# Kernel optimization log

Measured on AMD Instinct MI355X. Metric: run time of the kernel, lower is better.

The kernel has to match this reference:

```python
import jax, jax.numpy as jnp
import numpy as np

B, S, D, H = 8, 1024, 1024, 16
DH = D // H  # 64


def setup_inputs() -> dict:
    key0 = jax.random.key(0)
    ks = jax.random.split(key0, 12)
    mk = lambda k, shape: jax.random.normal(k, shape, dtype=jnp.float32)
    inp = {
        "key": mk(ks[0], (B, S, D)),
        "value": mk(ks[1], (B, S, D)),
        "query": mk(ks[2], (B, S, D)),
        "mask": jax.random.randint(ks[3], (B, S, S), 0, 2).astype(jnp.bool_),
        "Wq": mk(ks[4], (D, D)) * 0.02, "bq": jnp.zeros((D,), jnp.float32),
        "Wk": mk(ks[5], (D, D)) * 0.02, "bk": jnp.zeros((D,), jnp.float32),
        "Wv": mk(ks[6], (D, D)) * 0.02, "bv": jnp.zeros((D,), jnp.float32),
        "Wo": mk(ks[7], (D, D)) * 0.02, "bo": jnp.zeros((D,), jnp.float32),
    }
    return inp


def _split_heads(x):
    # [B, S, D] -> [B, H, S, DH]
    return x.reshape(B, -1, H, DH).transpose(0, 2, 1, 3)


def reference(key, value, query, mask, Wq, bq, Wk, bk, Wv, bv, Wo, bo):
    # linear projections (nn.Linear: x @ W.T + b)
    q = _split_heads(query @ Wq.T + bq) / jnp.sqrt(jnp.float32(DH))
    k = _split_heads(key @ Wk.T + bk)
    v = _split_heads(value @ Wv.T + bv)
    # scores: [B, H, Q, K]
    scores = jnp.einsum("bhqd,bhkd->bhqk", q, k)
    scores = jnp.where(mask[:, None, :, :], jnp.float32(-1e18), scores)
    attn = jax.nn.softmax(scores, axis=-1)
    # dropout is identity in eval mode (deterministic reference)
    ctx = jnp.einsum("bhqk,bhkd->bhqd", attn, v)
    ctx = ctx.transpose(0, 2, 1, 3).reshape(B, -1, D)
    out = ctx @ Wo.T + bo
    return out, attn
```

## Files before the change

### kernel.cpp

```cpp
#include <hip/hip_runtime.h>
#include <hip/hip_bf16.h>

#define BB 8
#define SS 1024
#define DD 1024
#define HH 16
#define DHH 64
#define MM (BB*SS)

typedef __attribute__((ext_vector_type(8))) short short8;
typedef __attribute__((ext_vector_type(4))) float f32x4;
typedef __fp16 half2v __attribute__((ext_vector_type(2)));
typedef __fp16 half8 __attribute__((ext_vector_type(8)));

typedef __attribute__((address_space(3))) void lds_void;
typedef const __attribute__((address_space(1))) void gbl_void;

__device__ __forceinline__ unsigned short f2bf(float f) {
  union { __hip_bfloat16 b; unsigned short u; } cv;
  cv.b = __float2bfloat16(f);
  return cv.u;
}
__device__ __forceinline__ float bf2f(unsigned short u) {
  return __builtin_bit_cast(float, (unsigned)u << 16);
}

__global__ void k_conv_w(const float* __restrict__ in, unsigned short* __restrict__ out,
                         float scale, int n8) {
  int i = blockIdx.x * blockDim.x + threadIdx.x;
  if (i >= n8) return;
  const float4* in4 = (const float4*)in;
  float4 a = in4[i * 2];
  float4 b = in4[i * 2 + 1];
  unsigned int w[4];
  w[0] = f2bf(a.x * scale) | ((unsigned)f2bf(a.y * scale) << 16);
  w[1] = f2bf(a.z * scale) | ((unsigned)f2bf(a.w * scale) << 16);
  w[2] = f2bf(b.x * scale) | ((unsigned)f2bf(b.y * scale) << 16);
  w[3] = f2bf(b.z * scale) | ((unsigned)f2bf(b.w * scale) << 16);
  *(uint4*)(out + (size_t)i * 8) = *(uint4*)w;
}

__global__ void k_detect_mask(const unsigned int* __restrict__ m, int* __restrict__ flag) {
  if (threadIdx.x || blockIdx.x) return;
  int i32 = 1, f32m = 1;
  for (int i = 0; i < 64; ++i) {
    unsigned v = m[i];
    if (v > 1u) i32 = 0;
    if (v != 0u && v != 0x3F800000u) f32m = 0;
  }
  *flag = i32 ? 0 : (f32m ? 1 : 2);
}

__global__ void k_maskbits(const void* __restrict__ mask, const int* __restrict__ mmode,
                           unsigned short* __restrict__ out) {
  int i = blockIdx.x * blockDim.x + threadIdx.x;
  if (i >= BB * 32 * 64 * 32) return;
  int r = i & 31, cb = (i >> 5) & 63, qb = (i >> 11) & 31, b = i >> 16;
  size_t src = ((size_t)(b * SS + qb * 32 + r) * SS) + cb * 16;
  int mm = *mmode;
  unsigned short bits = 0;
  if (mm == 2) {
    const unsigned char* p = (const unsigned char*)mask + src;
    uint4 v = *(const uint4*)p;
    const unsigned char* bytes = (const unsigned char*)&v;
#pragma unroll
    for (int c = 0; c < 16; c++) bits |= (bytes[c] ? 1u : 0u) << c;
  } else {
    const unsigned int* p = (const unsigned int*)mask + src;
#pragma unroll
    for (int q = 0; q < 4; q++) {
      uint4 v = *(const uint4*)(p + q * 4);
      bits |= (v.x ? 1u : 0u) << (q * 4 + 0);
      bits |= (v.y ? 1u : 0u) << (q * 4 + 1);
      bits |= (v.z ? 1u : 0u) << (q * 4 + 2);
      bits |= (v.w ? 1u : 0u) << (q * 4 + 3);
    }
  }
  out[i] = bits;
}

__global__ void __launch_bounds__(256, 2) k_gemm_qkv(
    const unsigned short* __restrict__ Xq, const unsigned short* __restrict__ Xk,
    const unsigned short* __restrict__ Xv,
    const unsigned short* __restrict__ Wqb, const unsigned short* __restrict__ Wkb,
    const unsigned short* __restrict__ Wvb,
    const float* __restrict__ bq, const float* __restrict__ bk, const float* __restrict__ bv,
    unsigned short* __restrict__ Oq, unsigned short* __restrict__ Ok,
    unsigned short* __restrict__ Ov) {
  int z = blockIdx.z;
  const unsigned short* A = (z == 0) ? Xq : (z == 1 ? Xk : Xv);
  const unsigned short* W = (z == 0) ? Wqb : (z == 1 ? Wkb : Wvb);
  const float* bias = (z == 0) ? bq : (z == 1 ? bk : bv);
  float bsc = (z == 0) ? 0.125f : 1.0f;
  unsigned short* O = (z == 0) ? Oq : (z == 1 ? Ok : Ov);

  __shared__ alignas(16) unsigned char As[128 * 64 * 2];
  __shared__ alignas(16) unsigned char Bs[128 * 64 * 2];

  int t = threadIdx.x;
  int row0 = blockIdx.y * 128, col0 = blockIdx.x * 128;
  int w = t >> 6, lane = t & 63, lr = lane & 15, lg = lane >> 4;
  int wm = w >> 1, wn = w & 1;

  int srow = w * 8 + (lane >> 3);
  int scol = (lane & 7) * 8;

  f32x4 z4 = {0.f, 0.f, 0.f, 0.f};
  f32x4 acc[4][4];
#pragma unroll
  for (int m = 0; m < 4; m++)
#pragma unroll
    for (int n = 0; n < 4; n++) acc[m][n] = z4;

  for (int kt = 0; kt < 16; ++kt) {
    int k0 = kt * 64;
#pragma unroll
    for (int i = 0; i < 4; ++i) {
      int r = i * 32 + srow;
      __builtin_amdgcn_global_load_lds(
          (gbl_void*)(A + (size_t)(row0 + r) * DD + k0 + scol),
          (lds_void*)(As + (i * 32 + w * 8) * 128), 16, 0, 0);
      __builtin_amdgcn_global_load_lds(
          (gbl_void*)(W + (size_t)(col0 + r) * DD + k0 + scol),
          (lds_void*)(Bs + (i * 32 + w * 8) * 128), 16, 0, 0);
    }
    __syncthreads();
#pragma unroll
    for (int kk = 0; kk < 2; ++kk) {
      short8 af[4], bfr[4];
#pragma unroll
      for (int m = 0; m < 4; m++) {
        int r = wm * 64 + m * 16 + lr;
        af[m] = *(const short8*)(As + r * 128 + kk * 64 + lg * 16);
      }
#pragma unroll
      for (int n = 0; n < 4; n++) {
        int r = wn * 64 + n * 16 + lr;
        bfr[n] = *(const short8*)(Bs + r * 128 + kk * 64 + lg * 16);
      }
#pragma unroll
      for (int m = 0; m < 4; m++)
#pragma unroll
        for (int n = 0; n < 4; n++)
          acc[m][n] = __builtin_amdgcn_mfma_f32_16x16x32_bf16(af[m], bfr[n], acc[m][n], 0, 0, 0);
    }
    __syncthreads();
  }
#pragma unroll
  for (int m = 0; m < 4; m++) {
#pragma unroll
    for (int n = 0; n < 4; n++) {
      int col = col0 + wn * 64 + n * 16 + lr;
      float bv_ = bias[col] * bsc;
#pragma unroll
      for (int j = 0; j < 4; j++) {
        int row = row0 + wm * 64 + m * 16 + lg * 4 + j;
        O[(size_t)row * DD + col] = f2bf(acc[m][n][j] + bv_);
      }
    }
  }
}

__global__ void __launch_bounds__(256, 2) k_gemm_out(
    const unsigned short* __restrict__ A, const unsigned short* __restrict__ W,
    const float* __restrict__ bias, float* __restrict__ Out) {
  __shared__ alignas(16) unsigned char As[128 * 64 * 2];
  __shared__ alignas(16) unsigned char Bs[128 * 64 * 2];

  int t = threadIdx.x;
  int row0 = blockIdx.y * 128, col0 = blockIdx.x * 128;
  int w = t >> 6, lane = t & 63, lr = lane & 15, lg = lane >> 4;
  int wm = w >> 1, wn = w & 1;

  int srow = w * 8 + (lane >> 3);
  int scol = (lane & 7) * 8;

  f32x4 z4 = {0.f, 0.f, 0.f, 0.f};
  f32x4 acc[4][4];
#pragma unroll
  for (int m = 0; m < 4; m++)
#pragma unroll
    for (int n = 0; n < 4; n++) acc[m][n] = z4;

  for (int kt = 0; kt < 16; ++kt) {
    int k0 = kt * 64;
#pragma unroll
    for (int i = 0; i < 4; ++i) {
      int r = i * 32 + srow;
      __builtin_amdgcn_global_load_lds(
          (gbl_void*)(A + (size_t)(row0 + r) * DD + k0 + scol),
          (lds_void*)(As + (i * 32 + w * 8) * 128), 16, 0, 0);
      __builtin_amdgcn_global_load_lds(
          (gbl_void*)(W + (size_t)(col0 + r) * DD + k0 + scol),
          (lds_void*)(Bs + (i * 32 + w * 8) * 128), 16, 0, 0);
    }
    __syncthreads();
#pragma unroll
    for (int kk = 0; kk < 2; ++kk) {
      short8 af[4], bfr[4];
#pragma unroll
      for (int m = 0; m < 4; m++) {
        int r = wm * 64 + m * 16 + lr;
        af[m] = *(const short8*)(As + r * 128 + kk * 64 + lg * 16);
      }
#pragma unroll
      for (int n = 0; n < 4; n++) {
        int r = wn * 64 + n * 16 + lr;
        bfr[n] = *(const short8*)(Bs + r * 128 + kk * 64 + lg * 16);
      }
#pragma unroll
      for (int m = 0; m < 4; m++)
#pragma unroll
        for (int n = 0; n < 4; n++)
          acc[m][n] = __builtin_amdgcn_mfma_f32_16x16x32_bf16(af[m], bfr[n], acc[m][n], 0, 0, 0);
    }
    __syncthreads();
  }
#pragma unroll
  for (int m = 0; m < 4; m++) {
#pragma unroll
    for (int n = 0; n < 4; n++) {
      int col = col0 + wn * 64 + n * 16 + lr;
      float bv_ = bias[col];
#pragma unroll
      for (int j = 0; j < 4; j++) {
        int row = row0 + wm * 64 + m * 16 + lg * 4 + j;
        Out[(size_t)row * DD + col] = acc[m][n][j] + bv_;
      }
    }
  }
}

__global__ void k_transpose_v(const unsigned short* __restrict__ V,
                              unsigned short* __restrict__ VT) {
  int blk = blockIdx.x;
  int s0 = (blk & 15) * 64;
  int h = (blk >> 4) & 15;
  int b = blk >> 8;
  __shared__ alignas(16) unsigned short T[64][72];
  int t = threadIdx.x;
  int rr = t >> 3, cc = t & 7;
#pragma unroll
  for (int p = 0; p < 2; p++) {
    int r = p * 32 + rr;
    uint4 v = *(const uint4*)(V + (size_t)(b * SS + s0 + r) * DD + h * 64 + cc * 8);
    *(uint4*)(&T[r][cc * 8]) = v;
  }
  __syncthreads();
#pragma unroll
  for (int p = 0; p < 2; p++) {
    int dh = p * 32 + rr;
    unsigned short tmp[8];
#pragma unroll
    for (int i = 0; i < 8; i++) tmp[i] = T[cc * 8 + i][dh];
    unsigned outw[4];
#pragma unroll
    for (int i = 0; i < 4; i++) {
      half2v hp = __builtin_amdgcn_cvt_pkrtz(bf2f(tmp[2 * i]), bf2f(tmp[2 * i + 1]));
      outw[i] = __builtin_bit_cast(unsigned, hp);
    }
    *(uint4*)(VT + (size_t)((b * HH + h) * DHH + dh) * SS + s0 + cc * 8) = *(uint4*)outw;
  }
}

__global__ void __launch_bounds__(256) k_attn(
    const unsigned short* __restrict__ Q, const unsigned short* __restrict__ K,
    const unsigned short* __restrict__ VT, const unsigned short* __restrict__ mbits,
    float* __restrict__ attn, unsigned short* __restrict__ ctx) {
  int wg = blockIdx.x;
  int xcd = wg & 7, idx = wg >> 3;
  int p_bh = xcd + (idx >> 5) * 8;
  int qb = idx & 31;
  int b = p_bh >> 4, h = p_bh & 15;
  int q0 = qb * 32;
  int t = threadIdx.x, w = t >> 6, lane = t & 63, lr = lane & 15, lg = lane >> 4;

  __shared__ float redsum[4][32];
  __shared__ alignas(16) unsigned char pbuf[24576];
  unsigned short (*P)[32][72] = (unsigned short(*)[32][72])pbuf;
  float (*cred)[32][64] = (float(*)[32][64])pbuf;

  short8 qf[2][2];
#pragma unroll
  for (int m = 0; m < 2; m++)
#pragma unroll
    for (int kb = 0; kb < 2; kb++)
      qf[m][kb] = *(const short8*)(Q + (size_t)(b * SS + q0 + m * 16 + lr) * DD +
                                   h * 64 + kb * 32 + lg * 8);

  const unsigned short* mb = mbits + (size_t)(b * 32 + qb) * 64 * 32;

  f32x4 z4 = {0.f, 0.f, 0.f, 0.f};
  float ps[2][4];
#pragma unroll
  for (int m = 0; m < 2; m++)
#pragma unroll
    for (int j = 0; j < 4; j++) ps[m][j] = 0.f;

  half2v scp[2][16][2];
#pragma unroll
  for (int c = 0; c < 16; c++) {
    int colb = w * 256 + c * 16;
    const unsigned short* kp = K + (size_t)(b * SS + colb + lr) * DD + h * 64 + lg * 8;
    short8 kf0 = *(const short8*)kp;
    short8 kf1 = *(const short8*)(kp + 32);
    int cb = w * 16 + c;
#pragma unroll
    for (int m = 0; m < 2; m++) {
      f32x4 s = __builtin_amdgcn_mfma_f32_16x16x32_bf16(qf[m][0], kf0, z4, 0, 0, 0);
      s = __builtin_amdgcn_mfma_f32_16x16x32_bf16(qf[m][1], kf1, s, 0, 0, 0);
      const unsigned short* mrow = mb + cb * 32 + m * 16 + lg * 4;
      ushort4 mw = *(const ushort4*)mrow;
      unsigned short mwa[4] = {mw.x, mw.y, mw.z, mw.w};
      float p[4];
#pragma unroll
      for (int j = 0; j < 4; j++)
        p[j] = ((mwa[j] >> lr) & 1) ? 0.0f : __expf(fminf(s[j], 10.0f));
      half2v h0 = __builtin_amdgcn_cvt_pkrtz(p[0], p[1]);
      half2v h1 = __builtin_amdgcn_cvt_pkrtz(p[2], p[3]);
      scp[m][c][0] = h0;
      scp[m][c][1] = h1;
      ps[m][0] += (float)h0[0];
      ps[m][1] += (float)h0[1];
      ps[m][2] += (float)h1[0];
      ps[m][3] += (float)h1[1];
    }
  }
#pragma unroll
  for (int m = 0; m < 2; m++)
#pragma unroll
    for (int j = 0; j < 4; j++) {
      float v = ps[m][j];
      v += __shfl_xor(v, 1);
      v += __shfl_xor(v, 2);
      v += __shfl_xor(v, 4);
      v += __shfl_xor(v, 8);
      ps[m][j] = v;
    }
  if (lr == 0) {
#pragma unroll
    for (int m = 0; m < 2; m++)
#pragma unroll
      for (int j = 0; j < 4; j++) redsum[w][m * 16 + lg * 4 + j] = ps[m][j];
  }
  __syncthreads();
  float inv[2][4];
#pragma unroll
  for (int m = 0; m < 2; m++)
#pragma unroll
    for (int j = 0; j < 4; j++) {
      int r = m * 16 + lg * 4 + j;
      inv[m][j] = 1.f / (redsum[0][r] + redsum[1][r] + redsum[2][r] + redsum[3][r]);
    }
  float invr[4];
#pragma unroll
  for (int rg = 0; rg < 4; rg++) {
    int r = rg * 8 + (lane >> 3);
    invr[rg] = 1.f / (redsum[0][r] + redsum[1][r] + redsum[2][r] + redsum[3][r]);
  }

  float* ab = attn + (size_t)((b * HH + h) * SS + q0) * SS;
  f32x4 cacc[2][4];
#pragma unroll
  for (int m = 0; m < 2; m++)
#pragma unroll
    for (int nb = 0; nb < 4; nb++) cacc[m][nb] = z4;

#pragma unroll
  for (int ch = 0; ch < 4; ch++) {
#pragma unroll
    for (int cc = 0; cc < 4; cc++) {
      int c = ch * 4 + cc;
      int col = cc * 16 + lr;
#pragma unroll
      for (int m = 0; m < 2; m++) {
        unsigned u0 = __builtin_bit_cast(unsigned, scp[m][c][0]);
        unsigned u1 = __builtin_bit_cast(unsigned, scp[m][c][1]);
        int r0 = m * 16 + lg * 4;
        P[w][r0 + 0][col] = (unsigned short)(u0 & 0xffffu);
        P[w][r0 + 1][col] = (unsigned short)(u0 >> 16);
        P[w][r0 + 2][col] = (unsigned short)(u1 & 0xffffu);
        P[w][r0 + 3][col] = (unsigned short)(u1 >> 16);
      }
    }
#pragma unroll
    for (int rg = 0; rg < 4; rg++) {
      int row = rg * 8 + (lane >> 3);
      float iv = invr[rg];
#pragma unroll
      for (int ci = 0; ci < 2; ci++) {
        int col = (lane & 7) * 4 + ci * 32;
        ushort4 hv = *(const ushort4*)(&P[w][row][col]);
        f32x4 o;
        o[0] = (float)__builtin_bit_cast(__fp16, hv.x) * iv;
        o[1] = (float)__builtin_bit_cast(__fp16, hv.y) * iv;
        o[2] = (float)__builtin_bit_cast(__fp16, hv.z) * iv;
        o[3] = (float)__builtin_bit_cast(__fp16, hv.w) * iv;
        __builtin_nontemporal_store(o, (f32x4*)(ab + (size_t)row * SS + w * 256 + ch * 64 + col));
      }
    }
#pragma unroll
    for (int kb = 0; kb < 2; kb++) {
      half8 vf[4];
#pragma unroll
      for (int nb = 0; nb < 4; nb++)
        vf[nb] = __builtin_bit_cast(half8,
            *(const short8*)(VT + (size_t)((b * HH + h) * DHH + nb * 16 + lr) * SS +
                             w * 256 + ch * 64 + kb * 32 + lg * 8));
      half8 pa[2];
#pragma unroll
      for (int m = 0; m < 2; m++)
        pa[m] = __builtin_bit_cast(half8, *(const short8*)(&P[w][m * 16 + lr][kb * 32 + lg * 8]));
#pragma unroll
      for (int m = 0; m < 2; m++)
#pragma unroll
        for (int nb = 0; nb < 4; nb++)
          cacc[m][nb] = __builtin_amdgcn_mfma_f32_16x16x32_f16(pa[m], vf[nb], cacc[m][nb], 0, 0, 0);
    }
  }
  __syncthreads();
  if (w > 0) {
#pragma unroll
    for (int m = 0; m < 2; m++)
#pragma unroll
      for (int nb = 0; nb < 4; nb++)
#pragma unroll
        for (int j = 0; j < 4; j++)
          cred[w - 1][m * 16 + lg * 4 + j][nb * 16 + lr] = cacc[m][nb][j];
  }
  __syncthreads();
  if (w == 0) {
#pragma unroll
    for (int m = 0; m < 2; m++)
#pragma unroll
      for (int nb = 0; nb < 4; nb++) {
        int col = nb * 16 + lr;
#pragma unroll
        for (int j = 0; j < 4; j++) {
          int rl = m * 16 + lg * 4 + j;
          float v = (cacc[m][nb][j] + cred[0][rl][col] + cred[1][rl][col] + cred[2][rl][col]) *
                    inv[m][j];
          ctx[(size_t)(b * SS + q0 + rl) * DD + h * 64 + col] = f2bf(v);
        }
      }
  }
}

extern "C" void kernel_launch(void* const* d_in, const int* in_sizes, int n_in,
                              void* d_out, int out_size, void* d_ws, size_t ws_size,
                              hipStream_t stream) {
  const float* key   = (const float*)d_in[0];
  const float* value = (const float*)d_in[1];
  const float* query = (const float*)d_in[2];
  const void*  mask  = d_in[3];
  const float* Wq = (const float*)d_in[4];
  const float* bq = (const float*)d_in[5];
  const float* Wk = (const float*)d_in[6];
  const float* bk = (const float*)d_in[7];
  const float* Wv = (const float*)d_in[8];
  const float* bv = (const float*)d_in[9];
  const float* Wo = (const float*)d_in[10];
  const float* bo = (const float*)d_in[11];

  unsigned short* wq_b = (unsigned short*)d_ws;
  unsigned short* wk_b = wq_b + (size_t)DD * DD;
  unsigned short* wv_b = wk_b + (size_t)DD * DD;
  unsigned short* wo_b = wv_b + (size_t)DD * DD;
  unsigned short* Qb   = wo_b + (size_t)DD * DD;
  unsigned short* Kb   = Qb + (size_t)MM * DD;
  unsigned short* Vb   = Kb + (size_t)MM * DD;
  unsigned short* VTb  = Vb + (size_t)MM * DD;
  unsigned short* CTXb = VTb + (size_t)MM * DD;
  unsigned short* MB   = CTXb + (size_t)MM * DD;
  int* flag = (int*)(MB + (size_t)BB * 32 * 64 * 32);
  size_t needed = (size_t)(4 * DD * DD + 5 * MM * DD) * 2 + (1u << 20) + 256;
  if (ws_size < needed) return;

  float* out  = (float*)d_out;
  float* attn = out + (size_t)MM * DD;

  unsigned short* Xq_b = (unsigned short*)attn;
  unsigned short* Xk_b = Xq_b + (size_t)MM * DD;
  unsigned short* Xv_b = Xk_b + (size_t)MM * DD;

  k_conv_w<<<512, 256, 0, stream>>>(Wq, wq_b, 0.125f, DD * DD / 8);
  k_conv_w<<<512, 256, 0, stream>>>(Wk, wk_b, 1.0f, DD * DD / 8);
  k_conv_w<<<512, 256, 0, stream>>>(Wv, wv_b, 1.0f, DD * DD / 8);
  k_conv_w<<<512, 256, 0, stream>>>(Wo, wo_b, 1.0f, DD * DD / 8);
  k_conv_w<<<4096, 256, 0, stream>>>(query, Xq_b, 1.0f, MM * DD / 8);
  k_conv_w<<<4096, 256, 0, stream>>>(key,   Xk_b, 1.0f, MM * DD / 8);
  k_conv_w<<<4096, 256, 0, stream>>>(value, Xv_b, 1.0f, MM * DD / 8);
  k_detect_mask<<<1, 1, 0, stream>>>((const unsigned int*)mask, flag);
  k_maskbits<<<2048, 256, 0, stream>>>(mask, flag, MB);
  k_gemm_qkv<<<dim3(8, 64, 3), 256, 0, stream>>>(Xq_b, Xk_b, Xv_b, wq_b, wk_b, wv_b,
                                                 bq, bk, bv, Qb, Kb, Vb);
  k_transpose_v<<<2048, 256, 0, stream>>>(Vb, VTb);
  k_attn<<<4096, 256, 0, stream>>>(Qb, Kb, VTb, MB, attn, CTXb);
  k_gemm_out<<<dim3(8, 64, 1), 256, 0, stream>>>(CTXb, wo_b, bo, out);
}
```

Measured before the change: 341.9 us.

## Fuse conversion launches, fold mask detection into maskbits, prefetch K tiles in attention

Merges the seven fp32-to-bf16 conversion launches into one kernel that routes each thread to its tensor by index. The single-thread mask-type detection kernel goes away: every maskbits block now redoes the 64-word check in shared memory. The attention score loop software-prefetches the next K fragment and mask words one iteration ahead. These target launch overhead and the serial detect kernel, and try to hide global-load latency in the attention kernel, at the cost of more registers in an already register-heavy loop.

```diff
diff --git a/kernel.cpp b/kernel.cpp
--- a/kernel.cpp
+++ b/kernel.cpp
@@ -25,10 +25,32 @@
   return __builtin_bit_cast(float, (unsigned)u << 16);
 }
 
-__global__ void k_conv_w(const float* __restrict__ in, unsigned short* __restrict__ out,
-                         float scale, int n8) {
-  int i = blockIdx.x * blockDim.x + threadIdx.x;
-  if (i >= n8) return;
+__global__ void k_conv_all(const float* __restrict__ Wq, const float* __restrict__ Wk,
+                           const float* __restrict__ Wv, const float* __restrict__ Wo,
+                           const float* __restrict__ Xq, const float* __restrict__ Xk,
+                           const float* __restrict__ Xv,
+                           unsigned short* __restrict__ owq, unsigned short* __restrict__ owk,
+                           unsigned short* __restrict__ owv, unsigned short* __restrict__ owo,
+                           unsigned short* __restrict__ oxq, unsigned short* __restrict__ oxk,
+                           unsigned short* __restrict__ oxv) {
+  int gi = blockIdx.x * blockDim.x + threadIdx.x;
+  const float* in;
+  unsigned short* out;
+  float scale = 1.0f;
+  int i;
+  if (gi < 524288) {
+    int z = gi >> 17;
+    i = gi & 131071;
+    in = (z == 0) ? Wq : (z == 1 ? Wk : (z == 2 ? Wv : Wo));
+    out = (z == 0) ? owq : (z == 1 ? owk : (z == 2 ? owv : owo));
+    if (z == 0) scale = 0.125f;
+  } else {
+    int gj = gi - 524288;
+    int z = gj >> 20;
+    i = gj & 1048575;
+    in = (z == 0) ? Xq : (z == 1 ? Xk : Xv);
+    out = (z == 0) ? oxq : (z == 1 ? oxk : oxv);
+  }
   const float4* in4 = (const float4*)in;
   float4 a = in4[i * 2];
   float4 b = in4[i * 2 + 1];
@@ -40,24 +62,24 @@
   *(uint4*)(out + (size_t)i * 8) = *(uint4*)w;
 }
 
-__global__ void k_detect_mask(const unsigned int* __restrict__ m, int* __restrict__ flag) {
-  if (threadIdx.x || blockIdx.x) return;
-  int i32 = 1, f32m = 1;
-  for (int i = 0; i < 64; ++i) {
-    unsigned v = m[i];
-    if (v > 1u) i32 = 0;
-    if (v != 0u && v != 0x3F800000u) f32m = 0;
-  }
-  *flag = i32 ? 0 : (f32m ? 1 : 2);
-}
-
-__global__ void k_maskbits(const void* __restrict__ mask, const int* __restrict__ mmode,
-                           unsigned short* __restrict__ out) {
+__global__ void k_maskbits(const void* __restrict__ mask, unsigned short* __restrict__ out) {
+  __shared__ int s_mm;
+  if (threadIdx.x == 0) {
+    const unsigned int* m = (const unsigned int*)mask;
+    int i32 = 1, f32m = 1;
+    for (int k = 0; k < 64; ++k) {
+      unsigned v = m[k];
+      if (v > 1u) i32 = 0;
+      if (v != 0u && v != 0x3F800000u) f32m = 0;
+    }
+    s_mm = i32 ? 0 : (f32m ? 1 : 2);
+  }
+  __syncthreads();
+  int mm = s_mm;
   int i = blockIdx.x * blockDim.x + threadIdx.x;
   if (i >= BB * 32 * 64 * 32) return;
   int r = i & 31, cb = (i >> 5) & 63, qb = (i >> 11) & 31, b = i >> 16;
   size_t src = ((size_t)(b * SS + qb * 32 + r) * SS) + cb * 16;
-  int mm = *mmode;
   unsigned short bits = 0;
   if (mm == 2) {
     const unsigned char* p = (const unsigned char*)mask + src;
@@ -298,20 +320,30 @@
     for (int j = 0; j < 4; j++) ps[m][j] = 0.f;
 
   half2v scp[2][16][2];
+  const unsigned short* kp0 = K + (size_t)(b * SS + w * 256 + lr) * DD + h * 64 + lg * 8;
+  short8 kf0 = *(const short8*)kp0;
+  short8 kf1 = *(const short8*)(kp0 + 32);
+  ushort4 mwc[2];
+  mwc[0] = *(const ushort4*)(mb + (w * 16) * 32 + lg * 4);
+  mwc[1] = *(const ushort4*)(mb + (w * 16) * 32 + 16 + lg * 4);
 #pragma unroll
   for (int c = 0; c < 16; c++) {
-    int colb = w * 256 + c * 16;
-    const unsigned short* kp = K + (size_t)(b * SS + colb + lr) * DD + h * 64 + lg * 8;
-    short8 kf0 = *(const short8*)kp;
-    short8 kf1 = *(const short8*)(kp + 32);
-    int cb = w * 16 + c;
+    short8 nkf0, nkf1;
+    ushort4 nmw0, nmw1;
+    if (c < 15) {
+      const unsigned short* np =
+          K + (size_t)(b * SS + w * 256 + (c + 1) * 16 + lr) * DD + h * 64 + lg * 8;
+      nkf0 = *(const short8*)np;
+      nkf1 = *(const short8*)(np + 32);
+      int ncb = w * 16 + c + 1;
+      nmw0 = *(const ushort4*)(mb + ncb * 32 + lg * 4);
+      nmw1 = *(const ushort4*)(mb + ncb * 32 + 16 + lg * 4);
+    }
 #pragma unroll
     for (int m = 0; m < 2; m++) {
       f32x4 s = __builtin_amdgcn_mfma_f32_16x16x32_bf16(qf[m][0], kf0, z4, 0, 0, 0);
       s = __builtin_amdgcn_mfma_f32_16x16x32_bf16(qf[m][1], kf1, s, 0, 0, 0);
-      const unsigned short* mrow = mb + cb * 32 + m * 16 + lg * 4;
-      ushort4 mw = *(const ushort4*)mrow;
-      unsigned short mwa[4] = {mw.x, mw.y, mw.z, mw.w};
+      unsigned short mwa[4] = {mwc[m].x, mwc[m].y, mwc[m].z, mwc[m].w};
       float p[4];
 #pragma unroll
       for (int j = 0; j < 4; j++)
@@ -324,6 +356,12 @@
       ps[m][1] += (float)h0[1];
       ps[m][2] += (float)h1[0];
       ps[m][3] += (float)h1[1];
+    }
+    if (c < 15) {
+      kf0 = nkf0;
+      kf1 = nkf1;
+      mwc[0] = nmw0;
+      mwc[1] = nmw1;
     }
   }
 #pragma unroll
@@ -472,7 +510,6 @@
   unsigned short* VTb  = Vb + (size_t)MM * DD;
   unsigned short* CTXb = VTb + (size_t)MM * DD;
   unsigned short* MB   = CTXb + (size_t)MM * DD;
-  int* flag = (int*)(MB + (size_t)BB * 32 * 64 * 32);
   size_t needed = (size_t)(4 * DD * DD + 5 * MM * DD) * 2 + (1u << 20) + 256;
   if (ws_size < needed) return;
 
@@ -483,15 +520,9 @@
   unsigned short* Xk_b = Xq_b + (size_t)MM * DD;
   unsigned short* Xv_b = Xk_b + (size_t)MM * DD;
 
-  k_conv_w<<<512, 256, 0, stream>>>(Wq, wq_b, 0.125f, DD * DD / 8);
-  k_conv_w<<<512, 256, 0, stream>>>(Wk, wk_b, 1.0f, DD * DD / 8);
-  k_conv_w<<<512, 256, 0, stream>>>(Wv, wv_b, 1.0f, DD * DD / 8);
-  k_conv_w<<<512, 256, 0, stream>>>(Wo, wo_b, 1.0f, DD * DD / 8);
-  k_conv_w<<<4096, 256, 0, stream>>>(query, Xq_b, 1.0f, MM * DD / 8);
-  k_conv_w<<<4096, 256, 0, stream>>>(key,   Xk_b, 1.0f, MM * DD / 8);
-  k_conv_w<<<4096, 256, 0, stream>>>(value, Xv_b, 1.0f, MM * DD / 8);
-  k_detect_mask<<<1, 1, 0, stream>>>((const unsigned int*)mask, flag);
-  k_maskbits<<<2048, 256, 0, stream>>>(mask, flag, MB);
+  k_conv_all<<<14336, 256, 0, stream>>>(Wq, Wk, Wv, Wo, query, key, value,
+                                        wq_b, wk_b, wv_b, wo_b, Xq_b, Xk_b, Xv_b);
+  k_maskbits<<<2048, 256, 0, stream>>>(mask, MB);
   k_gemm_qkv<<<dim3(8, 64, 3), 256, 0, stream>>>(Xq_b, Xk_b, Xv_b, wq_b, wk_b, wv_b,
                                                  bq, bk, bv, Qb, Kb, Vb);
   k_transpose_v<<<2048, 256, 0, stream>>>(Vb, VTb);
```

Result: faster. 321.9 us, median of 4 (-5.9%).
